# Kernel optimization log

Hardware: AMD Instinct MI355X
Metric: run time of the kernel (lower is better)

Reference implementation:

```python
import jax, jax.numpy as jnp
import numpy as np

B, N, D = 4, 1024, 1024   # batch, seq (x and context must match), model dim
H, DH = 16, 64            # heads, dim_head; inner_dim = H*DH = 1024
INNER = H * DH
EPS = 1e-5


def setup_inputs() -> dict:
    key = jax.random.key(0)
    ks = jax.random.split(key, 12)
    s = 0.02
    return {
        "x": jax.random.normal(ks[0], (B, N, D), dtype=jnp.float32),
        "context": jax.random.normal(ks[1], (B, N, D), dtype=jnp.float32),
        # weights stored as [in, out] (torch Linear weight transposed)
        "W_qk": jax.random.normal(ks[2], (D, INNER), dtype=jnp.float32) * s,
        "W_cqk": jax.random.normal(ks[3], (D, INNER), dtype=jnp.float32) * s,
        "W_v": jax.random.normal(ks[4], (D, INNER), dtype=jnp.float32) * s,
        "W_cv": jax.random.normal(ks[5], (D, INNER), dtype=jnp.float32) * s,
        "W_out": jax.random.normal(ks[6], (INNER, D), dtype=jnp.float32) * s,
        "b_out": jax.random.normal(ks[7], (D,), dtype=jnp.float32) * s,
        "W_cout": jax.random.normal(ks[8], (INNER, D), dtype=jnp.float32) * s,
        "b_cout": jax.random.normal(ks[9], (D,), dtype=jnp.float32) * s,
        "gamma": jnp.ones((D,), dtype=jnp.float32),
        "beta": jnp.zeros((D,), dtype=jnp.float32),
    }


def _split_heads(t):  # [b, n, h*d] -> [b, h, n, d]
    b, n, _ = t.shape
    return t.reshape(b, n, H, DH).transpose(0, 2, 1, 3)


def _merge_heads(t):  # [b, h, n, d] -> [b, n, h*d]
    b, h, n, d = t.shape
    return t.transpose(0, 2, 1, 3).reshape(b, n, h * d)


def _layernorm(y, gamma, beta):
    mu = jnp.mean(y, axis=-1, keepdims=True)
    var = jnp.var(y, axis=-1, keepdims=True)
    return gamma * (y - mu) * jax.lax.rsqrt(var + EPS) + beta


def reference(x, context, W_qk, W_cqk, W_v, W_cv, W_out, b_out, W_cout, b_cout, gamma, beta):
    scale = DH ** -0.5
    res = x + context                       # residual (requires identical shapes)
    # prenorm=False -> identity norms; dropout=0; talking_heads=False -> identity
    qk = _split_heads(x @ W_qk)             # [b,h,i,d]
    v = _split_heads(x @ W_v)               # [b,h,i,d]
    cqk = _split_heads(context @ W_cqk)     # [b,h,j,d]
    cv = _split_heads(context @ W_cv)       # [b,h,j,d]

    sim = jnp.einsum('bhid,bhjd->bhij', qk, cqk) * scale  # shared similarity
    attn = jax.nn.softmax(sim, axis=-1)      # row softmax (x attends to context)
    context_attn = jax.nn.softmax(sim, axis=-2)  # column softmax (context attends to x)

    out = jnp.einsum('bhij,bhjd->bhid', attn, cv)          # [b,h,i,d]
    context_out = jnp.einsum('bhji,bhjd->bhid', context_attn, v)  # [b,h,i,d]

    out = _merge_heads(out) @ W_out + b_out
    context_out = _merge_heads(context_out) @ W_cout + b_cout
    return _layernorm(out + context_out, gamma, beta) + res
```

## Files before the change

### kernel.cpp

```cpp
#include <hip/hip_runtime.h>
#include <hip/hip_bf16.h>

typedef unsigned short u16;
typedef __bf16 bf16x8 __attribute__((ext_vector_type(8)));
typedef float   f32x4 __attribute__((ext_vector_type(4)));
typedef u16     u16x8 __attribute__((ext_vector_type(8)));
typedef u16     u16x4 __attribute__((ext_vector_type(4)));

#define DEV static __device__ __forceinline__

DEV float bf2f(u16 b) { unsigned int u = ((unsigned int)b) << 16; return __builtin_bit_cast(float, u); }
DEV u16   f2bf(float f) { return __builtin_bit_cast(u16, (__bf16)f); }
DEV bf16x8 ldb(const u16* p) { return __builtin_bit_cast(bf16x8, *(const u16x8*)p); }

DEV f32x4 mfma_bf16(bf16x8 a, bf16x8 b, f32x4 c) {
  return __builtin_amdgcn_mfma_f32_16x16x32_bf16(a, b, c, 0, 0, 0);
}

DEV void gl16(const u16* g, u16* l) {
  __builtin_amdgcn_global_load_lds((const __attribute__((address_space(1))) unsigned int*)g,
                                   (__attribute__((address_space(3))) unsigned int*)l,
                                   16, 0, 0);
}

__global__ __launch_bounds__(256) void detect_dtype(const u16* x, int* flag) {
  int tid = threadIdx.x;
  u16 lo = x[tid * 2];
  float v = bf2f(lo);
  float av = fabsf(v);
  bool plaus = (av > 1e-4f && av < 50.f);
  __shared__ int cnt;
  if (tid == 0) cnt = 0;
  __syncthreads();
  if (plaus) atomicAdd(&cnt, 1);
  __syncthreads();
  if (tid == 0) *flag = (cnt >= 128) ? 1 : 0;
}

struct Cv2 { const void* s[2]; u16* d[2]; };
__global__ __launch_bounds__(256) void convert_big(Cv2 p, const int* flagp) {
  int fl = *flagp;
  const void* src = p.s[blockIdx.z];
  u16* dst = p.d[blockIdx.z];
  size_t i = ((size_t)blockIdx.x * 256 + threadIdx.x) * 8;
  if (fl) {
    *(u16x8*)(dst + i) = *(const u16x8*)((const u16*)src + i);
  } else {
    const float* s = (const float*)src + i;
    u16x8 o;
#pragma unroll
    for (int k = 0; k < 8; ++k) o[k] = f2bf(s[k]);
    *(u16x8*)(dst + i) = o;
  }
}

struct Sm4 { const void* s[4]; u16* d[4]; };
__global__ __launch_bounds__(256) void convert_smalls(Sm4 p, const int* flagp) {
  int fl = *flagp;
  const void* src = p.s[blockIdx.x];
  u16* dst = p.d[blockIdx.x];
  int i = threadIdx.x * 4;
#pragma unroll
  for (int k = 0; k < 4; ++k)
    dst[i + k] = fl ? ((const u16*)src)[i + k] : f2bf(((const float*)src)[i + k]);
}

struct T6 { const void* s[6]; u16* d[6]; };

__global__ __launch_bounds__(256) void transpose6(T6 t, const int* flagp) {
  int fl = *flagp;
  __shared__ u16 tile[32][33];
  const void* src = t.s[blockIdx.z];
  u16* dst = t.d[blockIdx.z];
  int x0 = blockIdx.x * 32, y0 = blockIdx.y * 32;
  int tx = threadIdx.x & 31, ty = threadIdx.x >> 5;
#pragma unroll
  for (int i = 0; i < 32; i += 8) {
    size_t idx = (size_t)(y0 + ty + i) * 1024 + x0 + tx;
    tile[ty + i][tx] = fl ? ((const u16*)src)[idx] : f2bf(((const float*)src)[idx]);
  }
  __syncthreads();
#pragma unroll
  for (int i = 0; i < 32; i += 8)
    dst[(size_t)(x0 + ty + i) * 1024 + y0 + tx] = tile[tx][ty + i];
}

struct Proj4 { const u16* A[4]; const u16* Bt[4]; u16* C[4]; int mode[4]; };

__global__ __launch_bounds__(256) void gemm_proj(Proj4 p) {
  const int K = 1024, Nn = 1024;
  const u16* A  = p.A[blockIdx.z];
  const u16* Bt = p.Bt[blockIdx.z];
  u16* C = p.C[blockIdx.z];
  int mode = p.mode[blockIdx.z];

  __shared__ __align__(16) u16 As[128 * 32];
  __shared__ __align__(16) u16 Bs[128 * 32];

  int tid = threadIdx.x, lane = tid & 63, w = tid >> 6;
  int wm = w & 1, wn = w >> 1;
  int q4 = lane >> 4, c = lane & 15;

  int bid = blockIdx.y * 8 + blockIdx.x;
  int wg  = (bid & 7) * 32 + (bid >> 3);
  int m0 = (wg >> 3) * 128, n0 = (wg & 7) * 128;

  int r0 = w * 32 + (lane >> 2);
  int cc = (lane & 3) ^ ((lane >> 3) & 3);
  const u16* pA0 = A  + (size_t)(m0 + r0) * K + cc * 8;
  const u16* pB0 = Bt + (size_t)(n0 + r0) * K + cc * 8;
  u16* lA0 = As + w * 1024;
  u16* lB0 = Bs + w * 1024;
  int qs = (q4 ^ ((c >> 1) & 3)) * 8;

  f32x4 acc[4][4] = {};

  for (int k0 = 0; k0 < K; k0 += 32) {
    __syncthreads();
    gl16(pA0 + k0,                  lA0);
    gl16(pA0 + (size_t)16 * K + k0, lA0 + 512);
    gl16(pB0 + k0,                  lB0);
    gl16(pB0 + (size_t)16 * K + k0, lB0 + 512);
    asm volatile("s_waitcnt vmcnt(0)" ::: "memory");
    __syncthreads();
    bf16x8 af[4], bfr[4];
#pragma unroll
    for (int i = 0; i < 4; ++i) af[i]  = ldb(As + (wm * 64 + i * 16 + c) * 32 + qs);
#pragma unroll
    for (int j = 0; j < 4; ++j) bfr[j] = ldb(Bs + (wn * 64 + j * 16 + c) * 32 + qs);
#pragma unroll
    for (int i = 0; i < 4; ++i)
#pragma unroll
      for (int j = 0; j < 4; ++j)
        acc[i][j] = mfma_bf16(af[i], bfr[j], acc[i][j]);
  }

  if (mode == 0) {
#pragma unroll
    for (int i = 0; i < 4; ++i) {
      int mrow = m0 + wm * 64 + i * 16 + q4 * 4;
#pragma unroll
      for (int j = 0; j < 4; ++j) {
        int col = n0 + wn * 64 + j * 16 + c;
#pragma unroll
        for (int r = 0; r < 4; ++r)
          C[(size_t)(mrow + r) * Nn + col] = f2bf(acc[i][j][r]);
      }
    }
  } else {
    int bidx = m0 >> 10;
#pragma unroll
    for (int i = 0; i < 4; ++i) {
      int mrow = m0 + wm * 64 + i * 16 + q4 * 4;
      int jj = mrow & 1023;
#pragma unroll
      for (int j = 0; j < 4; ++j) {
        int col = n0 + wn * 64 + j * 16 + c;
        int h = col >> 6, dh = col & 63;
        u16x4 pk;
#pragma unroll
        for (int r = 0; r < 4; ++r) pk[r] = f2bf(acc[i][j][r]);
        *(u16x4*)(C + ((size_t)((bidx * 16 + h) * 64 + dh)) * 1024 + jj) = pk;
      }
    }
  }
}

__global__ __launch_bounds__(256) void flash_attn(const u16* Q, const u16* Kg,
                                                  const u16* Vt, u16* O) {
  int bh = blockIdx.y; int b = bh >> 4, h = bh & 15;
  int i0 = blockIdx.x * 64;
  int tid = threadIdx.x, lane = tid & 63, w = tid >> 6;
  int q4 = lane >> 4, c = lane & 15;

  __shared__ __align__(16) u16 Ks[64 * 72];
  __shared__ __align__(16) u16 Vs[64 * 72];
  __shared__ __align__(16) u16 Ps[4][16 * 72];

  const size_t qoff = ((size_t)(b * 1024 + i0 + w * 16 + c)) * 1024 + h * 64 + q4 * 8;
  bf16x8 qf0 = ldb(Q + qoff);
  bf16x8 qf1 = ldb(Q + qoff + 32);

  f32x4 of[4] = {};
  f32x4 lacc = {};
  bf16x8 ones;
#pragma unroll
  for (int k = 0; k < 8; ++k) ones[k] = (__bf16)1.0f;

  int jr = tid >> 2, seg = (tid & 3) * 16;
  const u16* krow_base = Kg + ((size_t)(b * 1024 + jr)) * 1024 + h * 64 + seg;
  const u16* vrow_base = Vt + ((size_t)((b * 16 + h) * 64 + jr)) * 1024 + seg;
  const float scale = 0.125f;

  for (int j0 = 0; j0 < 1024; j0 += 64) {
    const u16* ks = krow_base + (size_t)j0 * 1024;
    u16x8 kv0 = *(const u16x8*)(ks);
    u16x8 kv1 = *(const u16x8*)(ks + 8);
    const u16* vs = vrow_base + j0;
    u16x8 vv0 = *(const u16x8*)(vs);
    u16x8 vv1 = *(const u16x8*)(vs + 8);
    __syncthreads();
    *(u16x8*)(Ks + jr * 72 + seg)     = kv0;
    *(u16x8*)(Ks + jr * 72 + seg + 8) = kv1;
    *(u16x8*)(Vs + jr * 72 + seg)     = vv0;
    *(u16x8*)(Vs + jr * 72 + seg + 8) = vv1;
    __syncthreads();

    f32x4 sf[4] = {};
#pragma unroll
    for (int jc = 0; jc < 4; ++jc) {
      bf16x8 k0f = ldb(Ks + (jc * 16 + c) * 72 + q4 * 8);
      bf16x8 k1f = ldb(Ks + (jc * 16 + c) * 72 + 32 + q4 * 8);
      sf[jc] = mfma_bf16(k0f, qf0, sf[jc]);
      sf[jc] = mfma_bf16(k1f, qf1, sf[jc]);
    }

#pragma unroll
    for (int jc = 0; jc < 4; ++jc) {
      u16x4 pk;
#pragma unroll
      for (int r = 0; r < 4; ++r) {
        float s = fminf(fmaxf(sf[jc][r] * scale, -60.f), 60.f);
        pk[r] = f2bf(__expf(s));
      }
      *(u16x4*)(Ps[w] + c * 72 + jc * 16 + q4 * 4) = pk;
    }

    asm volatile("s_waitcnt lgkmcnt(0)" ::: "memory");

    bf16x8 pf0 = ldb(Ps[w] + c * 72 + q4 * 8);
    bf16x8 pf1 = ldb(Ps[w] + c * 72 + 32 + q4 * 8);

    lacc = mfma_bf16(pf0, ones, lacc);
    lacc = mfma_bf16(pf1, ones, lacc);

#pragma unroll
    for (int dc = 0; dc < 4; ++dc) {
      bf16x8 v0f = ldb(Vs + (dc * 16 + c) * 72 + q4 * 8);
      bf16x8 v1f = ldb(Vs + (dc * 16 + c) * 72 + 32 + q4 * 8);
      of[dc] = mfma_bf16(pf0, v0f, of[dc]);
      of[dc] = mfma_bf16(pf1, v1f, of[dc]);
    }
  }

  float inv[4];
#pragma unroll
  for (int r = 0; r < 4; ++r) inv[r] = 1.0f / lacc[r];
#pragma unroll
  for (int dc = 0; dc < 4; ++dc) {
    int col = h * 64 + dc * 16 + c;
#pragma unroll
    for (int r = 0; r < 4; ++r) {
      int irow = i0 + w * 16 + q4 * 4 + r;
      O[((size_t)(b * 1024 + irow)) * 1024 + col] = f2bf(of[dc][r] * inv[r]);
    }
  }
}

__global__ __launch_bounds__(256) void gemm_final(const u16* A1, const u16* B1t,
                                                  const u16* A2, const u16* B2t,
                                                  const u16* b1, const u16* b2,
                                                  float* Y) {
  const int K = 1024, Nn = 1024;
  __shared__ __align__(16) u16 As[128 * 32];
  __shared__ __align__(16) u16 Bs[128 * 32];

  int tid = threadIdx.x, lane = tid & 63, w = tid >> 6;
  int wm = w & 1, wn = w >> 1;
  int q4 = lane >> 4, c = lane & 15;

  int bid = blockIdx.y * 8 + blockIdx.x;
  int wg  = (bid & 7) * 32 + (bid >> 3);
  int m0 = (wg >> 3) * 128, n0 = (wg & 7) * 128;

  int r0 = w * 32 + (lane >> 2);
  int cc = (lane & 3) ^ ((lane >> 3) & 3);
  const u16* A1p = A1  + (size_t)(m0 + r0) * K + cc * 8;
  const u16* A2p = A2  + (size_t)(m0 + r0) * K + cc * 8;
  const u16* B1p = B1t + (size_t)(n0 + r0) * K + cc * 8;
  const u16* B2p = B2t + (size_t)(n0 + r0) * K + cc * 8;
  u16* lA0 = As + w * 1024;
  u16* lB0 = Bs + w * 1024;
  int qs = (q4 ^ ((c >> 1) & 3)) * 8;

  f32x4 acc[4][4] = {};

  for (int kk = 0; kk < 64; ++kk) {
    const u16* Ap = (kk < 32) ? A1p : A2p;
    const u16* Bp = (kk < 32) ? B1p : B2p;
    int k0 = (kk & 31) * 32;
    __syncthreads();
    gl16(Ap + k0,                  lA0);
    gl16(Ap + (size_t)16 * K + k0, lA0 + 512);
    gl16(Bp + k0,                  lB0);
    gl16(Bp + (size_t)16 * K + k0, lB0 + 512);
    asm volatile("s_waitcnt vmcnt(0)" ::: "memory");
    __syncthreads();
    bf16x8 af[4], bfr[4];
#pragma unroll
    for (int i = 0; i < 4; ++i) af[i]  = ldb(As + (wm * 64 + i * 16 + c) * 32 + qs);
#pragma unroll
    for (int j = 0; j < 4; ++j) bfr[j] = ldb(Bs + (wn * 64 + j * 16 + c) * 32 + qs);
#pragma unroll
    for (int i = 0; i < 4; ++i)
#pragma unroll
      for (int j = 0; j < 4; ++j)
        acc[i][j] = mfma_bf16(af[i], bfr[j], acc[i][j]);
  }

#pragma unroll
  for (int i = 0; i < 4; ++i) {
    int mrow = m0 + wm * 64 + i * 16 + q4 * 4;
#pragma unroll
    for (int j = 0; j < 4; ++j) {
      int col = n0 + wn * 64 + j * 16 + c;
      float bias = bf2f(b1[col]) + bf2f(b2[col]);
#pragma unroll
      for (int r = 0; r < 4; ++r)
        Y[(size_t)(mrow + r) * Nn + col] = acc[i][j][r] + bias;
    }
  }
}

__global__ __launch_bounds__(256) void ln_res(const float* Y, const u16* gamma, const u16* beta,
                                              const u16* x, const u16* ctx, void* out,
                                              const int* flagp) {
  int fl = *flagp;
  int row = blockIdx.x;
  int tid = threadIdx.x;
  const float* y = Y + (size_t)row * 1024;
  float4 v = *(const float4*)(y + tid * 4);
  float s  = v.x + v.y + v.z + v.w;
  float s2 = v.x * v.x + v.y * v.y + v.z * v.z + v.w * v.w;
#pragma unroll
  for (int off = 1; off < 64; off <<= 1) { s += __shfl_xor(s, off); s2 += __shfl_xor(s2, off); }
  __shared__ float red[8];
  int w = tid >> 6, lane = tid & 63;
  if (lane == 0) { red[w] = s; red[w + 4] = s2; }
  __syncthreads();
  float S  = red[0] + red[1] + red[2] + red[3];
  float S2 = red[4] + red[5] + red[6] + red[7];
  float mu  = S * (1.0f / 1024.0f);
  float var = S2 * (1.0f / 1024.0f) - mu * mu;
  float rs = rsqrtf(var + 1e-5f);
  size_t base = (size_t)row * 1024 + tid * 4;
  u16x4 gv = *(const u16x4*)(gamma + tid * 4);
  u16x4 bv = *(const u16x4*)(beta + tid * 4);
  u16x4 xv = *(const u16x4*)(x + base);
  u16x4 cv = *(const u16x4*)(ctx + base);
  float vv[4] = {v.x, v.y, v.z, v.w};
  float o[4];
#pragma unroll
  for (int k = 0; k < 4; ++k)
    o[k] = bf2f(gv[k]) * (vv[k] - mu) * rs + bf2f(bv[k]) + bf2f(xv[k]) + bf2f(cv[k]);
  if (fl) {
    u16x4 ov;
#pragma unroll
    for (int k = 0; k < 4; ++k) ov[k] = f2bf(o[k]);
    *(u16x4*)((u16*)out + base) = ov;
  } else {
    *(float4*)((float*)out + base) = make_float4(o[0], o[1], o[2], o[3]);
  }
}

__global__ __launch_bounds__(256) void sentinel(u16* out) {
  size_t i = ((size_t)blockIdx.x * 256 + threadIdx.x) * 8;
  u16 v = f2bf(12345.0f);
  u16x8 o = {v, v, v, v, v, v, v, v};
  *(u16x8*)(out + i) = o;
}

extern "C" void kernel_launch(void* const* d_in, const int* in_sizes, int n_in,
                              void* d_out, int out_size, void* d_ws, size_t ws_size,
                              hipStream_t stream) {
  (void)in_sizes; (void)n_in; (void)out_size;
  const size_t MB = 1024 * 1024;
  const size_t NEED = 61 * MB;
  if (ws_size < NEED) {
    sentinel<<<2048, 256, 0, stream>>>((u16*)d_out);
    return;
  }

  char* ws = (char*)d_ws;
  u16* wt[6];
  for (int i = 0; i < 6; ++i) wt[i] = (u16*)(ws + (size_t)i * 2 * MB);
  u16* xc   = (u16*)(ws + 12 * MB);
  u16* cc   = (u16*)(ws + 20 * MB);
  u16* qk   = (u16*)(ws + 28 * MB);
  u16* cqk  = (u16*)(ws + 36 * MB);
  u16* vt   = (u16*)(ws + 44 * MB);
  u16* cvt  = (u16*)(ws + 52 * MB);
  u16* oa   = (u16*)(ws + 0);
  u16* ca   = (u16*)(ws + 52 * MB);
  float* y  = (float*)(ws + 28 * MB);
  int* flag = (int*)(ws + 60 * MB);
  u16* b1c  = (u16*)(ws + 60 * MB + 4096);
  u16* b2c  = (u16*)(ws + 60 * MB + 8192);
  u16* gc   = (u16*)(ws + 60 * MB + 12288);
  u16* bc   = (u16*)(ws + 60 * MB + 16384);

  detect_dtype<<<1, 256, 0, stream>>>((const u16*)d_in[0], flag);

  Cv2 cv;
  cv.s[0] = d_in[0]; cv.d[0] = xc;
  cv.s[1] = d_in[1]; cv.d[1] = cc;
  convert_big<<<dim3(2048, 1, 2), 256, 0, stream>>>(cv, flag);

  Sm4 sm;
  sm.s[0] = d_in[7]; sm.d[0] = b1c;
  sm.s[1] = d_in[9]; sm.d[1] = b2c;
  sm.s[2] = d_in[10]; sm.d[2] = gc;
  sm.s[3] = d_in[11]; sm.d[3] = bc;
  convert_smalls<<<4, 256, 0, stream>>>(sm, flag);

  T6 t;
  t.s[0] = d_in[2]; t.d[0] = wt[0];
  t.s[1] = d_in[3]; t.d[1] = wt[1];
  t.s[2] = d_in[4]; t.d[2] = wt[2];
  t.s[3] = d_in[5]; t.d[3] = wt[3];
  t.s[4] = d_in[6]; t.d[4] = wt[4];
  t.s[5] = d_in[8]; t.d[5] = wt[5];
  transpose6<<<dim3(32, 32, 6), 256, 0, stream>>>(t, flag);

  Proj4 p;
  p.A[0] = xc; p.Bt[0] = wt[0]; p.C[0] = qk;  p.mode[0] = 0;
  p.A[1] = cc; p.Bt[1] = wt[1]; p.C[1] = cqk; p.mode[1] = 0;
  p.A[2] = xc; p.Bt[2] = wt[2]; p.C[2] = vt;  p.mode[2] = 1;
  p.A[3] = cc; p.Bt[3] = wt[3]; p.C[3] = cvt; p.mode[3] = 1;
  gemm_proj<<<dim3(8, 32, 4), 256, 0, stream>>>(p);

  flash_attn<<<dim3(16, 64), 256, 0, stream>>>(qk, cqk, cvt, oa);
  flash_attn<<<dim3(16, 64), 256, 0, stream>>>(cqk, qk, vt, ca);

  gemm_final<<<dim3(8, 32), 256, 0, stream>>>(oa, wt[4], ca, wt[5], b1c, b2c, y);

  ln_res<<<4096, 256, 0, stream>>>(y, gc, bc, xc, cc, d_out, flag);
}
```

Before: 292.8 us.

## Double-buffer GEMM LDS tiles and prefetch attention K/V into registers

The projection and output GEMMs now use two LDS buffers per operand. The next K-slice is issued with global_load_lds while the current slice feeds the MFMAs, and the explicit vmcnt(0) wait is dropped, leaving load-completion ordering to the compiler and the barriers. The attention kernel loads the next K/V tile into registers right after storing the current one to LDS, so global latency overlaps the score and PV MFMAs. It also raises wave priority around the MFMA blocks. The cost is double the GEMM LDS footprint, which may reduce occupancy, and correctness depends on the compiler inserting the right waits for the asynchronous LDS loads.

```diff
diff --git a/kernel.cpp b/kernel.cpp
--- a/kernel.cpp
+++ b/kernel.cpp
@@ -94,8 +94,8 @@
   u16* C = p.C[blockIdx.z];
   int mode = p.mode[blockIdx.z];
 
-  __shared__ __align__(16) u16 As[128 * 32];
-  __shared__ __align__(16) u16 Bs[128 * 32];
+  __shared__ __align__(16) u16 As[2][128 * 32];
+  __shared__ __align__(16) u16 Bs[2][128 * 32];
 
   int tid = threadIdx.x, lane = tid & 63, w = tid >> 6;
   int wm = w & 1, wn = w >> 1;
@@ -109,31 +109,38 @@
   int cc = (lane & 3) ^ ((lane >> 3) & 3);
   const u16* pA0 = A  + (size_t)(m0 + r0) * K + cc * 8;
   const u16* pB0 = Bt + (size_t)(n0 + r0) * K + cc * 8;
-  u16* lA0 = As + w * 1024;
-  u16* lB0 = Bs + w * 1024;
   int qs = (q4 ^ ((c >> 1) & 3)) * 8;
 
   f32x4 acc[4][4] = {};
 
-  for (int k0 = 0; k0 < K; k0 += 32) {
-    __syncthreads();
-    gl16(pA0 + k0,                  lA0);
-    gl16(pA0 + (size_t)16 * K + k0, lA0 + 512);
-    gl16(pB0 + k0,                  lB0);
-    gl16(pB0 + (size_t)16 * K + k0, lB0 + 512);
-    asm volatile("s_waitcnt vmcnt(0)" ::: "memory");
-    __syncthreads();
-    bf16x8 af[4], bfr[4];
-#pragma unroll
-    for (int i = 0; i < 4; ++i) af[i]  = ldb(As + (wm * 64 + i * 16 + c) * 32 + qs);
-#pragma unroll
-    for (int j = 0; j < 4; ++j) bfr[j] = ldb(Bs + (wn * 64 + j * 16 + c) * 32 + qs);
-#pragma unroll
-    for (int i = 0; i < 4; ++i)
-#pragma unroll
-      for (int j = 0; j < 4; ++j)
-        acc[i][j] = mfma_bf16(af[i], bfr[j], acc[i][j]);
-  }
+#define STAGE_P(buf, koff)                                        \
+  { gl16(pA0 + (koff),          As[buf] + w * 1024);              \
+    gl16(pA0 + 16 * K + (koff), As[buf] + w * 1024 + 512);        \
+    gl16(pB0 + (koff),          Bs[buf] + w * 1024);              \
+    gl16(pB0 + 16 * K + (koff), Bs[buf] + w * 1024 + 512); }
+
+#define COMP_P(buf)                                               \
+  { bf16x8 af[4], bfr[4];                                         \
+    _Pragma("unroll") for (int i = 0; i < 4; ++i)                 \
+      af[i]  = ldb(As[buf] + (wm * 64 + i * 16 + c) * 32 + qs);   \
+    _Pragma("unroll") for (int j = 0; j < 4; ++j)                 \
+      bfr[j] = ldb(Bs[buf] + (wn * 64 + j * 16 + c) * 32 + qs);   \
+    _Pragma("unroll") for (int i = 0; i < 4; ++i)                 \
+      _Pragma("unroll") for (int j = 0; j < 4; ++j)               \
+        acc[i][j] = mfma_bf16(af[i], bfr[j], acc[i][j]); }
+
+  STAGE_P(0, 0);
+  __syncthreads();
+  for (int k0 = 0; k0 < K; k0 += 64) {
+    STAGE_P(1, k0 + 32);
+    COMP_P(0);
+    __syncthreads();
+    if (k0 + 64 < K) STAGE_P(0, k0 + 64);
+    COMP_P(1);
+    __syncthreads();
+  }
+#undef STAGE_P
+#undef COMP_P
 
   if (mode == 0) {
 #pragma unroll
@@ -192,13 +199,12 @@
   const u16* vrow_base = Vt + ((size_t)((b * 16 + h) * 64 + jr)) * 1024 + seg;
   const float scale = 0.125f;
 
+  u16x8 kv0 = *(const u16x8*)(krow_base);
+  u16x8 kv1 = *(const u16x8*)(krow_base + 8);
+  u16x8 vv0 = *(const u16x8*)(vrow_base);
+  u16x8 vv1 = *(const u16x8*)(vrow_base + 8);
+
   for (int j0 = 0; j0 < 1024; j0 += 64) {
-    const u16* ks = krow_base + (size_t)j0 * 1024;
-    u16x8 kv0 = *(const u16x8*)(ks);
-    u16x8 kv1 = *(const u16x8*)(ks + 8);
-    const u16* vs = vrow_base + j0;
-    u16x8 vv0 = *(const u16x8*)(vs);
-    u16x8 vv1 = *(const u16x8*)(vs + 8);
     __syncthreads();
     *(u16x8*)(Ks + jr * 72 + seg)     = kv0;
     *(u16x8*)(Ks + jr * 72 + seg + 8) = kv1;
@@ -206,7 +212,17 @@
     *(u16x8*)(Vs + jr * 72 + seg + 8) = vv1;
     __syncthreads();
 
+    if (j0 + 64 < 1024) {
+      const u16* ks = krow_base + (size_t)(j0 + 64) * 1024;
+      kv0 = *(const u16x8*)(ks);
+      kv1 = *(const u16x8*)(ks + 8);
+      const u16* vs = vrow_base + j0 + 64;
+      vv0 = *(const u16x8*)(vs);
+      vv1 = *(const u16x8*)(vs + 8);
+    }
+
     f32x4 sf[4] = {};
+    __builtin_amdgcn_s_setprio(1);
 #pragma unroll
     for (int jc = 0; jc < 4; ++jc) {
       bf16x8 k0f = ldb(Ks + (jc * 16 + c) * 72 + q4 * 8);
@@ -214,6 +230,7 @@
       sf[jc] = mfma_bf16(k0f, qf0, sf[jc]);
       sf[jc] = mfma_bf16(k1f, qf1, sf[jc]);
     }
+    __builtin_amdgcn_s_setprio(0);
 
 #pragma unroll
     for (int jc = 0; jc < 4; ++jc) {
@@ -234,6 +251,7 @@
     lacc = mfma_bf16(pf0, ones, lacc);
     lacc = mfma_bf16(pf1, ones, lacc);
 
+    __builtin_amdgcn_s_setprio(1);
 #pragma unroll
     for (int dc = 0; dc < 4; ++dc) {
       bf16x8 v0f = ldb(Vs + (dc * 16 + c) * 72 + q4 * 8);
@@ -241,6 +259,7 @@
       of[dc] = mfma_bf16(pf0, v0f, of[dc]);
       of[dc] = mfma_bf16(pf1, v1f, of[dc]);
     }
+    __builtin_amdgcn_s_setprio(0);
   }
 
   float inv[4];
@@ -262,8 +281,8 @@
                                                   const u16* b1, const u16* b2,
                                                   float* Y) {
   const int K = 1024, Nn = 1024;
-  __shared__ __align__(16) u16 As[128 * 32];
-  __shared__ __align__(16) u16 Bs[128 * 32];
+  __shared__ __align__(16) u16 As[2][128 * 32];
+  __shared__ __align__(16) u16 Bs[2][128 * 32];
 
   int tid = threadIdx.x, lane = tid & 63, w = tid >> 6;
   int wm = w & 1, wn = w >> 1;
@@ -279,34 +298,41 @@
   const u16* A2p = A2  + (size_t)(m0 + r0) * K + cc * 8;
   const u16* B1p = B1t + (size_t)(n0 + r0) * K + cc * 8;
   const u16* B2p = B2t + (size_t)(n0 + r0) * K + cc * 8;
-  u16* lA0 = As + w * 1024;
-  u16* lB0 = Bs + w * 1024;
   int qs = (q4 ^ ((c >> 1) & 3)) * 8;
 
   f32x4 acc[4][4] = {};
 
-  for (int kk = 0; kk < 64; ++kk) {
-    const u16* Ap = (kk < 32) ? A1p : A2p;
-    const u16* Bp = (kk < 32) ? B1p : B2p;
-    int k0 = (kk & 31) * 32;
-    __syncthreads();
-    gl16(Ap + k0,                  lA0);
-    gl16(Ap + (size_t)16 * K + k0, lA0 + 512);
-    gl16(Bp + k0,                  lB0);
-    gl16(Bp + (size_t)16 * K + k0, lB0 + 512);
-    asm volatile("s_waitcnt vmcnt(0)" ::: "memory");
-    __syncthreads();
-    bf16x8 af[4], bfr[4];
-#pragma unroll
-    for (int i = 0; i < 4; ++i) af[i]  = ldb(As + (wm * 64 + i * 16 + c) * 32 + qs);
-#pragma unroll
-    for (int j = 0; j < 4; ++j) bfr[j] = ldb(Bs + (wn * 64 + j * 16 + c) * 32 + qs);
-#pragma unroll
-    for (int i = 0; i < 4; ++i)
-#pragma unroll
-      for (int j = 0; j < 4; ++j)
-        acc[i][j] = mfma_bf16(af[i], bfr[j], acc[i][j]);
-  }
+#define STAGE_F(buf, kk)                                          \
+  { const u16* Ap = ((kk) < 32) ? A1p : A2p;                      \
+    const u16* Bp = ((kk) < 32) ? B1p : B2p;                      \
+    int k0_ = ((kk) & 31) * 32;                                   \
+    gl16(Ap + k0_,          As[buf] + w * 1024);                  \
+    gl16(Ap + 16 * K + k0_, As[buf] + w * 1024 + 512);            \
+    gl16(Bp + k0_,          Bs[buf] + w * 1024);                  \
+    gl16(Bp + 16 * K + k0_, Bs[buf] + w * 1024 + 512); }
+
+#define COMP_F(buf)                                               \
+  { bf16x8 af[4], bfr[4];                                         \
+    _Pragma("unroll") for (int i = 0; i < 4; ++i)                 \
+      af[i]  = ldb(As[buf] + (wm * 64 + i * 16 + c) * 32 + qs);   \
+    _Pragma("unroll") for (int j = 0; j < 4; ++j)                 \
+      bfr[j] = ldb(Bs[buf] + (wn * 64 + j * 16 + c) * 32 + qs);   \
+    _Pragma("unroll") for (int i = 0; i < 4; ++i)                 \
+      _Pragma("unroll") for (int j = 0; j < 4; ++j)               \
+        acc[i][j] = mfma_bf16(af[i], bfr[j], acc[i][j]); }
+
+  STAGE_F(0, 0);
+  __syncthreads();
+  for (int kk = 0; kk < 64; kk += 2) {
+    STAGE_F(1, kk + 1);
+    COMP_F(0);
+    __syncthreads();
+    if (kk + 2 < 64) STAGE_F(0, kk + 2);
+    COMP_F(1);
+    __syncthreads();
+  }
+#undef STAGE_F
+#undef COMP_F
 
 #pragma unroll
   for (int i = 0; i < 4; ++i) {
```

Result: no change. 298.0 us (+1.8%).
